# Optimization experiments

Measured on AMD Instinct MI355X. Metric: run time of the kernel, lower is better.

Reference implementation:

```python
import jax, jax.numpy as jnp
import numpy as np

# Module config
T = 4.0          # distillation temperature (init arg)
NUM_BINS = 256   # number of unique quantized feature values present in the tensors
N, C, H, W = 64, 256, 32, 32
EPS = 1e-8


def setup_inputs() -> dict:
    key = jax.random.key(0)
    k1, k2 = jax.random.split(key)
    # Quantized features: integer-valued floats in [0, NUM_BINS). All 256 levels
    # appear w.h.p., so torch.unique(features).sort()[0] == arange(NUM_BINS).
    feat_s = jax.random.randint(k1, (N, C, H, W), 0, NUM_BINS).astype(jnp.float32)
    feat_t = jax.random.randint(k2, (N, C, H, W), 0, NUM_BINS).astype(jnp.float32)
    return {"feat_s": feat_s, "feat_t": feat_t}


def _feature_to_prob(features):
    # Replaces the original per-unique-value Python loop with one fused
    # scatter-add histogram. Values are exact integers, so equality-compare
    # counting == bincount on the integer cast.
    b = features.shape[0]
    idx = features.reshape(b, -1).astype(jnp.int32)              # [N, C*H*W]
    hist = jnp.zeros((b, NUM_BINS), jnp.float32)
    hist = hist.at[jnp.arange(b)[:, None], idx].add(1.0)         # [N, NUM_BINS]
    return jnp.log(hist + EPS)


def reference(feat_s, feat_t):
    prob_s = _feature_to_prob(feat_s)
    prob_t = _feature_to_prob(feat_t)
    p_s = jax.nn.log_softmax(prob_s / T, axis=1)                 # log-probs
    p_t = jax.nn.softmax(prob_t / T, axis=1)                     # probs
    # F.kl_div(log_input=p_s, target=p_t, size_average=False) = sum p_t*(log p_t - p_s)
    kl = jnp.sum(p_t * (jnp.log(p_t) - p_s))
    loss = kl * (T ** 2) / feat_s.shape[0]
    return loss
```

## Files before the change

kernel.cpp:

```cpp
#include <hip/hip_runtime.h>

#define NBATCH   64
#define BINS     256
#define PER_BATCH (256 * 32 * 32)
#define CHUNKS   16
#define THREADS  256
#define F4_PER_CHUNK (PER_BATCH / 4 / CHUNKS)
#define F4_PER_THREAD (F4_PER_CHUNK / THREADS)

__global__ __launch_bounds__(THREADS) void hist_kernel(
    const float* __restrict__ fs, const float* __restrict__ ft,
    int* __restrict__ ghist) {
  __shared__ int sh[4][BINS];
  const int tid = threadIdx.x;

  for (int i = tid; i < 4 * BINS; i += THREADS) ((int*)sh)[i] = 0;
  __syncthreads();

  const int tb    = blockIdx.x >> 4;
  const int chunk = blockIdx.x & 15;
  const float* src  = (tb < NBATCH) ? fs : ft;
  const int    batch = tb & (NBATCH - 1);

  const float4* p = (const float4*)(src + (size_t)batch * PER_BATCH)
                    + (size_t)chunk * F4_PER_CHUNK;
  const int w = tid >> 6;

#pragma unroll
  for (int i = 0; i < F4_PER_THREAD; ++i) {
    float4 v = p[(size_t)i * THREADS + tid];
    atomicAdd(&sh[w][((int)v.x) & 255], 1);
    atomicAdd(&sh[w][((int)v.y) & 255], 1);
    atomicAdd(&sh[w][((int)v.z) & 255], 1);
    atomicAdd(&sh[w][((int)v.w) & 255], 1);
  }
  __syncthreads();

  int total = sh[0][tid] + sh[1][tid] + sh[2][tid] + sh[3][tid];
  if (total) atomicAdd(&ghist[tb * BINS + tid], total);
}

__global__ __launch_bounds__(1024) void kl_kernel(
    const int* __restrict__ ghist, float* __restrict__ out) {
  __shared__ double wacc[16];
  const int tid  = threadIdx.x;
  const int wave = tid >> 6;
  const int lane = tid & 63;

  double acc = 0.0;
  for (int n = wave; n < NBATCH; n += 16) {
    const int* hs = ghist + n * BINS;
    const int* ht = ghist + (NBATCH + n) * BINS;

    double ls[4], lt[4];
#pragma unroll
    for (int j = 0; j < 4; ++j) {
      const int bin = lane + 64 * j;
      ls[j] = log((double)hs[bin] + 1e-8) * 0.25;
      lt[j] = log((double)ht[bin] + 1e-8) * 0.25;
    }

    double ms = ls[0], mt = lt[0];
#pragma unroll
    for (int j = 1; j < 4; ++j) { ms = fmax(ms, ls[j]); mt = fmax(mt, lt[j]); }
    for (int off = 32; off; off >>= 1) {
      ms = fmax(ms, __shfl_xor(ms, off));
      mt = fmax(mt, __shfl_xor(mt, off));
    }

    double ss = 0.0, st = 0.0;
#pragma unroll
    for (int j = 0; j < 4; ++j) { ss += exp(ls[j] - ms); st += exp(lt[j] - mt); }
    for (int off = 32; off; off >>= 1) {
      ss += __shfl_xor(ss, off);
      st += __shfl_xor(st, off);
    }
    const double lse_s = ms + log(ss);
    const double lse_t = mt + log(st);

    double term = 0.0;
#pragma unroll
    for (int j = 0; j < 4; ++j) {
      const double lpt = lt[j] - lse_t;
      const double lps = ls[j] - lse_s;
      term += exp(lpt) * (lpt - lps);
    }
    for (int off = 32; off; off >>= 1) term += __shfl_xor(term, off);

    if (lane == 0) acc += term;
  }

  if (lane == 0) wacc[wave] = acc;
  __syncthreads();
  if (tid == 0) {
    double t = 0.0;
    for (int i = 0; i < 16; ++i) t += wacc[i];
    out[0] = (float)(t * 0.25);
  }
}

extern "C" void kernel_launch(void* const* d_in, const int* in_sizes, int n_in,
                              void* d_out, int out_size, void* d_ws, size_t ws_size,
                              hipStream_t stream) {
  const float* fs = (const float*)d_in[0];
  const float* ft = (const float*)d_in[1];
  int* ghist = (int*)d_ws;

  hipMemsetAsync(d_ws, 0, (size_t)2 * NBATCH * BINS * sizeof(int), stream);

  hist_kernel<<<dim3(128 * CHUNKS), dim3(THREADS), 0, stream>>>(fs, ft, ghist);
  kl_kernel<<<dim3(1), dim3(1024), 0, stream>>>(ghist, (float*)d_out);
}
```

Before: 184.1 us.

## Use per-thread packed 8-bit shared histograms and split KL across blocks

The histogram kernel now gives each thread its own private sub-histogram in shared memory, packing four 8-bit counters per 32-bit word. This removes shared-atomic contention between lanes; each thread handles 128 values, so the byte counters cannot overflow. The reduction reads the packed words with a rotating index to avoid bank conflicts, unpacks them into 16-bit lanes and combines them with shuffles. Chunks per batch drop from 16 to 8, and the single-block KL kernel is split into a 64-block per-batch kernel plus a finalize kernel, at the cost of a 64KB shared footprint that limits occupancy and one extra launch.

New measurement: 169.6 us. 7.9% less time.

```diff
diff --git a/kernel.cpp b/kernel.cpp
--- a/kernel.cpp
+++ b/kernel.cpp
@@ -1,102 +1,106 @@
 #include <hip/hip_runtime.h>
 
-#define NBATCH   64
-#define BINS     256
+#define NBATCH    64
+#define BINS      256
 #define PER_BATCH (256 * 32 * 32)
-#define CHUNKS   16
-#define THREADS  256
-#define F4_PER_CHUNK (PER_BATCH / 4 / CHUNKS)
-#define F4_PER_THREAD (F4_PER_CHUNK / THREADS)
+#define THREADS   256
+#define CHUNKS    8
+#define F4_PER_THREAD 32
+#define F4_PER_CHUNK  (F4_PER_THREAD * THREADS)
 
 __global__ __launch_bounds__(THREADS) void hist_kernel(
     const float* __restrict__ fs, const float* __restrict__ ft,
     int* __restrict__ ghist) {
-  __shared__ int sh[4][BINS];
+  __shared__ unsigned sh[64 * THREADS];
   const int tid = threadIdx.x;
 
-  for (int i = tid; i < 4 * BINS; i += THREADS) ((int*)sh)[i] = 0;
-  __syncthreads();
+#pragma unroll
+  for (int g = 0; g < 64; ++g) sh[g * THREADS + tid] = 0u;
 
-  const int tb    = blockIdx.x >> 4;
-  const int chunk = blockIdx.x & 15;
-  const float* src  = (tb < NBATCH) ? fs : ft;
+  const int tb    = blockIdx.x >> 3;
+  const int chunk = blockIdx.x & 7;
+  const float* src   = (tb < NBATCH) ? fs : ft;
   const int    batch = tb & (NBATCH - 1);
-
   const float4* p = (const float4*)(src + (size_t)batch * PER_BATCH)
                     + (size_t)chunk * F4_PER_CHUNK;
-  const int w = tid >> 6;
 
-#pragma unroll
+#pragma unroll 8
   for (int i = 0; i < F4_PER_THREAD; ++i) {
-    float4 v = p[(size_t)i * THREADS + tid];
-    atomicAdd(&sh[w][((int)v.x) & 255], 1);
-    atomicAdd(&sh[w][((int)v.y) & 255], 1);
-    atomicAdd(&sh[w][((int)v.z) & 255], 1);
-    atomicAdd(&sh[w][((int)v.w) & 255], 1);
+    float4 v = p[i * THREADS + tid];
+    int b0 = (int)v.x, b1 = (int)v.y, b2 = (int)v.z, b3 = (int)v.w;
+    atomicAdd(&sh[((b0 >> 2) << 8) + tid], 1u << ((b0 & 3) << 3));
+    atomicAdd(&sh[((b1 >> 2) << 8) + tid], 1u << ((b1 & 3) << 3));
+    atomicAdd(&sh[((b2 >> 2) << 8) + tid], 1u << ((b2 & 3) << 3));
+    atomicAdd(&sh[((b3 >> 2) << 8) + tid], 1u << ((b3 & 3) << 3));
   }
   __syncthreads();
 
-  int total = sh[0][tid] + sh[1][tid] + sh[2][tid] + sh[3][tid];
-  if (total) atomicAdd(&ghist[tb * BINS + tid], total);
+  const int g = tid >> 2;
+  const unsigned qbase = (unsigned)g * THREADS + (unsigned)(tid & 3) * 64u;
+  unsigned acc0 = 0, acc1 = 0;
+#pragma unroll 4
+  for (int j = 0; j < 64; ++j) {
+    unsigned w = sh[qbase + ((j + tid) & 63)];
+    acc0 += w & 0x00FF00FFu;
+    acc1 += (w >> 8) & 0x00FF00FFu;
+  }
+  acc0 += __shfl_xor(acc0, 1);  acc0 += __shfl_xor(acc0, 2);
+  acc1 += __shfl_xor(acc1, 1);  acc1 += __shfl_xor(acc1, 2);
+
+  const int sub = tid & 3;
+  unsigned cnt = (((sub & 1) ? acc1 : acc0) >> ((sub & 2) * 8)) & 0xFFFFu;
+  atomicAdd(&ghist[tb * BINS + tid], (int)cnt);
 }
 
-__global__ __launch_bounds__(1024) void kl_kernel(
-    const int* __restrict__ ghist, float* __restrict__ out) {
-  __shared__ double wacc[16];
-  const int tid  = threadIdx.x;
-  const int wave = tid >> 6;
-  const int lane = tid & 63;
+__global__ __launch_bounds__(256) void kl_batch(
+    const int* __restrict__ ghist, double* __restrict__ partial) {
+  __shared__ double reda[4], redb[4];
+  const int n = blockIdx.x, tid = threadIdx.x;
+  const int w = tid >> 6, lane = tid & 63;
+  const int* hs = ghist + n * BINS;
+  const int* ht = ghist + (NBATCH + n) * BINS;
 
-  double acc = 0.0;
-  for (int n = wave; n < NBATCH; n += 16) {
-    const int* hs = ghist + n * BINS;
-    const int* ht = ghist + (NBATCH + n) * BINS;
+  double ls = log((double)hs[tid] + 1e-8) * 0.25;
+  double lt = log((double)ht[tid] + 1e-8) * 0.25;
 
-    double ls[4], lt[4];
-#pragma unroll
-    for (int j = 0; j < 4; ++j) {
-      const int bin = lane + 64 * j;
-      ls[j] = log((double)hs[bin] + 1e-8) * 0.25;
-      lt[j] = log((double)ht[bin] + 1e-8) * 0.25;
-    }
+  double ms = ls, mt = lt;
+  for (int off = 32; off; off >>= 1) {
+    ms = fmax(ms, __shfl_xor(ms, off));
+    mt = fmax(mt, __shfl_xor(mt, off));
+  }
+  if (lane == 0) { reda[w] = ms; redb[w] = mt; }
+  __syncthreads();
+  ms = fmax(fmax(reda[0], reda[1]), fmax(reda[2], reda[3]));
+  mt = fmax(fmax(redb[0], redb[1]), fmax(redb[2], redb[3]));
+  __syncthreads();
 
-    double ms = ls[0], mt = lt[0];
-#pragma unroll
-    for (int j = 1; j < 4; ++j) { ms = fmax(ms, ls[j]); mt = fmax(mt, lt[j]); }
-    for (int off = 32; off; off >>= 1) {
-      ms = fmax(ms, __shfl_xor(ms, off));
-      mt = fmax(mt, __shfl_xor(mt, off));
-    }
+  double ss = exp(ls - ms), st = exp(lt - mt);
+  for (int off = 32; off; off >>= 1) {
+    ss += __shfl_xor(ss, off);
+    st += __shfl_xor(st, off);
+  }
+  if (lane == 0) { reda[w] = ss; redb[w] = st; }
+  __syncthreads();
+  ss = reda[0] + reda[1] + reda[2] + reda[3];
+  st = redb[0] + redb[1] + redb[2] + redb[3];
+  const double lse_s = ms + log(ss);
+  const double lse_t = mt + log(st);
 
-    double ss = 0.0, st = 0.0;
-#pragma unroll
-    for (int j = 0; j < 4; ++j) { ss += exp(ls[j] - ms); st += exp(lt[j] - mt); }
-    for (int off = 32; off; off >>= 1) {
-      ss += __shfl_xor(ss, off);
-      st += __shfl_xor(st, off);
-    }
-    const double lse_s = ms + log(ss);
-    const double lse_t = mt + log(st);
+  const double lpt = lt - lse_t;
+  const double lps = ls - lse_s;
+  double term = exp(lpt) * (lpt - lps);
+  for (int off = 32; off; off >>= 1) term += __shfl_xor(term, off);
+  __syncthreads();
+  if (lane == 0) reda[w] = term;
+  __syncthreads();
+  if (tid == 0) partial[n] = reda[0] + reda[1] + reda[2] + reda[3];
+}
 
-    double term = 0.0;
-#pragma unroll
-    for (int j = 0; j < 4; ++j) {
-      const double lpt = lt[j] - lse_t;
-      const double lps = ls[j] - lse_s;
-      term += exp(lpt) * (lpt - lps);
-    }
-    for (int off = 32; off; off >>= 1) term += __shfl_xor(term, off);
-
-    if (lane == 0) acc += term;
-  }
-
-  if (lane == 0) wacc[wave] = acc;
-  __syncthreads();
-  if (tid == 0) {
-    double t = 0.0;
-    for (int i = 0; i < 16; ++i) t += wacc[i];
-    out[0] = (float)(t * 0.25);
-  }
+__global__ __launch_bounds__(64) void finalize(
+    const double* __restrict__ partial, float* __restrict__ out) {
+  double v = partial[threadIdx.x];
+  for (int off = 32; off; off >>= 1) v += __shfl_xor(v, off);
+  if (threadIdx.x == 0) out[0] = (float)(v * 0.25);
 }
 
 extern "C" void kernel_launch(void* const* d_in, const int* in_sizes, int n_in,
@@ -104,10 +108,12 @@
                               hipStream_t stream) {
   const float* fs = (const float*)d_in[0];
   const float* ft = (const float*)d_in[1];
-  int* ghist = (int*)d_ws;
+  int*    ghist   = (int*)d_ws;
+  double* partial = (double*)((char*)d_ws + 2 * NBATCH * BINS * sizeof(int));
 
   hipMemsetAsync(d_ws, 0, (size_t)2 * NBATCH * BINS * sizeof(int), stream);
 
   hist_kernel<<<dim3(128 * CHUNKS), dim3(THREADS), 0, stream>>>(fs, ft, ghist);
-  kl_kernel<<<dim3(1), dim3(1024), 0, stream>>>(ghist, (float*)d_out);
+  kl_batch<<<dim3(NBATCH), dim3(256), 0, stream>>>(ghist, partial);
+  finalize<<<dim3(1), dim3(64), 0, stream>>>(partial, (float*)d_out);
 }
```
